# Kernel tuning notes

Measured on AMD Instinct MI355X. Metric: run time of the kernel, lower is better.

The kernel has to match this reference:

```python
import jax, jax.numpy as jnp
import numpy as np

N_NODES = 50000
N_EDGES = 800000
NUM_GRAPHS = 256
IN = 128
HID = 256
NUM_CLASSES = 10
EPS = 1e-5


def _glorot(key, shape):
    fan_in, fan_out = shape[0], shape[1]
    lim = (6.0 / (fan_in + fan_out)) ** 0.5
    return jax.random.uniform(key, shape, jnp.float32, -lim, lim)


def setup_inputs() -> dict:
    key = jax.random.key(0)
    ks = jax.random.split(key, 32)
    x = jax.random.normal(ks[0], (N_NODES, IN), jnp.float32)
    edge_index = jax.random.randint(ks[1], (2, N_EDGES), 0, N_NODES, jnp.int64)
    batch = jnp.sort(jax.random.randint(ks[2], (N_NODES,), 0, NUM_GRAPHS, jnp.int64))
    h = IN // 2  # 64
    p = {
        "x": x, "edge_index": edge_index, "batch": batch,
        # SAGEConv: out = lin_l(mean_aggr(x_j)) + lin_r(x_i); lin_l has bias, lin_r none
        "W1l": _glorot(ks[3], (IN, h)), "b1l": jnp.zeros((h,), jnp.float32), "W1r": _glorot(ks[4], (IN, h)),
        "W2l": _glorot(ks[5], (h, h)), "b2l": jnp.zeros((h,), jnp.float32), "W2r": _glorot(ks[6], (h, h)),
        "W3l": _glorot(ks[7], (h, h)), "b3l": jnp.zeros((h,), jnp.float32), "W3r": _glorot(ks[8], (h, h)),
        "lin1_w": _glorot(ks[9], (h, HID)), "lin1_b": jnp.zeros((HID,), jnp.float32),
        "g1": jnp.ones((HID,), jnp.float32), "be1": jnp.zeros((HID,), jnp.float32),
        "lin2_w": _glorot(ks[10], (HID, HID // 2)), "lin2_b": jnp.zeros((HID // 2,), jnp.float32),
        "g2": jnp.ones((HID // 2,), jnp.float32), "be2": jnp.zeros((HID // 2,), jnp.float32),
        "lin3_w": _glorot(ks[11], (HID // 2, HID // 4)), "lin3_b": jnp.zeros((HID // 4,), jnp.float32),
        "g3": jnp.ones((HID // 4,), jnp.float32), "be3": jnp.zeros((HID // 4,), jnp.float32),
        "lin4_w": _glorot(ks[12], (HID // 4, NUM_CLASSES)), "lin4_b": jnp.zeros((NUM_CLASSES,), jnp.float32),
    }
    return p


def sage_conv(x, src, dst, Wl, bl, Wr):
    # mean aggregation of source-node messages at destination nodes
    msg = x[src]  # [E, d] gather
    agg = jax.ops.segment_sum(msg, dst, num_segments=N_NODES)
    cnt = jax.ops.segment_sum(jnp.ones((src.shape[0],), x.dtype), dst, num_segments=N_NODES)
    agg = agg / jnp.maximum(cnt, 1.0)[:, None]
    return agg @ Wl + bl + x @ Wr


def batch_norm(x, gamma, beta):
    # training-mode BN (batch statistics, biased variance) as in torch default
    mean = jnp.mean(x, axis=0)
    var = jnp.mean((x - mean) ** 2, axis=0)
    return (x - mean) / jnp.sqrt(var + EPS) * gamma + beta


def reference(x, edge_index, batch,
              W1l, b1l, W1r, W2l, b2l, W2r, W3l, b3l, W3r,
              lin1_w, lin1_b, g1, be1, lin2_w, lin2_b, g2, be2,
              lin3_w, lin3_b, g3, be3, lin4_w, lin4_b):
    src, dst = edge_index[0], edge_index[1]
    h = sage_conv(x, src, dst, W1l, b1l, W1r)
    h = sage_conv(h, src, dst, W2l, b2l, W2r)
    h = sage_conv(h, src, dst, W3l, b3l, W3r)
    # global_mean_pool over graphs
    s = jax.ops.segment_sum(h, batch, num_segments=NUM_GRAPHS)
    n = jax.ops.segment_sum(jnp.ones((h.shape[0],), h.dtype), batch, num_segments=NUM_GRAPHS)
    c = s / jnp.maximum(n, 1.0)[:, None]
    # dropout is identity (self.training = False)
    c = jnp.tanh(batch_norm(c @ lin1_w + lin1_b, g1, be1))
    c = jnp.tanh(batch_norm(c @ lin2_w + lin2_b, g2, be2))
    c = jnp.tanh(batch_norm(c @ lin3_w + lin3_b, g3, be3))
    return c @ lin4_w + lin4_b
```

## Files before the change

### kernel.cpp

```cpp
#include <hip/hip_runtime.h>
#include <hip/hip_bf16.h>

#define N_NODES   50000
#define N_EDGES   800000
#define NUM_GRAPHS 256
#define IN_DIM    128
#define HD        64
#define EPS       1e-5f
#define SCAN_NB   196
#define NB_HEAD   64

typedef __hip_bfloat16 bf16;

__global__ void k_diag(float* __restrict__ out, int n, float v) {
    int t = blockIdx.x * 256 + threadIdx.x;
    if (t < n) out[t] = v;
}

__global__ void k_count(const int* __restrict__ dst, const int* __restrict__ batch,
                        int* __restrict__ cnti, int* __restrict__ pos,
                        int* __restrict__ gb) {
    int e = blockIdx.x * 256 + threadIdx.x;
    if (e < N_EDGES) pos[e] = atomicAdd(&cnti[dst[e]], 1);
    if (e < N_NODES) {
        int bg = batch[e];
        int bnext = (e + 1 < N_NODES) ? batch[e + 1] : NUM_GRAPHS;
        if (e == 0) {
            for (int g = 0; g <= bg; ++g) gb[g] = 0;
        }
        for (int g = bg + 1; g <= bnext; ++g) gb[g] = e + 1;
    }
}

__global__ void k_scan1(const int* __restrict__ cnti, int* __restrict__ off,
                        int* __restrict__ bsum) {
    __shared__ int wsum[4];
    int idx = blockIdx.x * 256 + threadIdx.x;
    int lane = threadIdx.x & 63, wid = threadIdx.x >> 6;
    int v = (idx < N_NODES) ? cnti[idx] : 0;
    int s = v;
    #pragma unroll
    for (int o = 1; o < 64; o <<= 1) {
        int u = __shfl_up(s, o);
        if (lane >= o) s += u;
    }
    if (lane == 63) wsum[wid] = s;
    __syncthreads();
    int wbase = 0;
    #pragma unroll
    for (int w = 0; w < 4; w++) wbase += (w < wid) ? wsum[w] : 0;
    if (idx < N_NODES) off[idx] = wbase + s - v;
    if (threadIdx.x == 255) bsum[blockIdx.x] = wbase + s;
}

__global__ void k_scan3(int* __restrict__ off, const int* __restrict__ bsum,
                        const int* __restrict__ gb, float* __restrict__ invc) {
    __shared__ int wsum[4];
    __shared__ int spre;
    int lane = threadIdx.x & 63, wid = threadIdx.x >> 6;
    int v = (threadIdx.x < blockIdx.x) ? bsum[threadIdx.x] : 0;
    #pragma unroll
    for (int o = 32; o > 0; o >>= 1) v += __shfl_down(v, o);
    if (lane == 0) wsum[wid] = v;
    __syncthreads();
    if (threadIdx.x == 0) spre = wsum[0] + wsum[1] + wsum[2] + wsum[3];
    __syncthreads();
    int pre = spre;
    int idx = blockIdx.x * 256 + threadIdx.x;
    if (idx < N_NODES) off[idx] += pre;
    else if (idx == N_NODES) off[N_NODES] = N_EDGES;
    if (blockIdx.x == 0 && threadIdx.x < NUM_GRAPHS) {
        int c0 = gb[threadIdx.x], c1 = gb[threadIdx.x + 1];
        invc[threadIdx.x] = 1.0f / (float)max(c1 - c0, 1);
    }
}

__global__ void k_fill(const int* __restrict__ src, const int* __restrict__ dst,
                       const int* __restrict__ off, const int* __restrict__ pos,
                       int* __restrict__ nbr) {
    int e = blockIdx.x * 256 + threadIdx.x;
    if (e >= N_EDGES) return;
    int d = dst[e];
    nbr[off[d] + pos[e]] = src[e];
}

template <int K>
__global__ __launch_bounds__(256) void k_xform3(
        const float* __restrict__ X, const float* __restrict__ Wl,
        const float* __restrict__ Wr, const float* __restrict__ bl,
        bf16* __restrict__ B, float* __restrict__ C) {
    __shared__ float tile[32 * K];
    const int NPW = 8;
    int nodes0 = blockIdx.x * 32;
    {
        const int total4 = 32 * K / 4;
        int nmax4 = (N_NODES - nodes0) * K / 4;
        const float4* Xg = (const float4*)(X + (long)nodes0 * K);
        float4* tg = (float4*)tile;
        for (int idx = threadIdx.x; idx < total4; idx += 256) {
            float4 v = make_float4(0.f, 0.f, 0.f, 0.f);
            if (idx < nmax4) v = Xg[idx];
            tg[idx] = v;
        }
    }
    __syncthreads();
    int wave = threadIdx.x >> 6, j = threadIdx.x & 63;
    long base = (long)nodes0 + wave * NPW;
    if (base >= N_NODES) return;
    float accB[NPW], accC[NPW];
    #pragma unroll
    for (int n = 0; n < NPW; n++) { accB[n] = 0.f; accC[n] = 0.f; }
    const float* Xs = tile + (wave * NPW) * K;
    for (int kc = 0; kc < K; kc += 4) {
        float wl0 = Wl[(kc + 0) * HD + j], wr0 = Wr[(kc + 0) * HD + j];
        float wl1 = Wl[(kc + 1) * HD + j], wr1 = Wr[(kc + 1) * HD + j];
        float wl2 = Wl[(kc + 2) * HD + j], wr2 = Wr[(kc + 2) * HD + j];
        float wl3 = Wl[(kc + 3) * HD + j], wr3 = Wr[(kc + 3) * HD + j];
        #pragma unroll
        for (int n = 0; n < NPW; n++) {
            float4 xv = *(const float4*)(Xs + n * K + kc);
            accB[n] = fmaf(xv.x, wl0, accB[n]);
            accC[n] = fmaf(xv.x, wr0, accC[n]);
            accB[n] = fmaf(xv.y, wl1, accB[n]);
            accC[n] = fmaf(xv.y, wr1, accC[n]);
            accB[n] = fmaf(xv.z, wl2, accB[n]);
            accC[n] = fmaf(xv.z, wr2, accC[n]);
            accB[n] = fmaf(xv.w, wl3, accB[n]);
            accC[n] = fmaf(xv.w, wr3, accC[n]);
        }
    }
    float bb = bl[j];
    int nact = (int)min((long)NPW, (long)N_NODES - base);
    for (int n = 0; n < nact; n++) {
        long i = base + n;
        B[i * HD + j] = __float2bfloat16(accB[n]);
        C[i * HD + j] = accC[n] + bb;
    }
}

__device__ __forceinline__ float bflo(unsigned u) { return __uint_as_float(u << 16); }
__device__ __forceinline__ float bfhi(unsigned u) { return __uint_as_float(u & 0xffff0000u); }

template <bool LAST>
__global__ void k_gather(const int* __restrict__ off, const int* __restrict__ nbr,
                         const bf16* __restrict__ Bm, float* __restrict__ C,
                         const int* __restrict__ batch, const float* __restrict__ invc,
                         float* __restrict__ cb) {
    int t = blockIdx.x * 256 + threadIdx.x;
    int i = t >> 6, lane = t & 63;
    if (!LAST && i >= N_NODES) return;
    int half = lane >> 5, c = lane & 31;
    int wid = threadIdx.x >> 6;
    const unsigned* B2 = (const unsigned*)Bm;
    int beg = off[i], end = off[i + 1];
    float e0 = 0.f, e1 = 0.f, e2 = 0.f, e3 = 0.f;
    float e4 = 0.f, e5 = 0.f, e6 = 0.f, e7 = 0.f;
    float o0 = 0.f, o1 = 0.f, o2 = 0.f, o3 = 0.f;
    float o4 = 0.f, o5 = 0.f, o6 = 0.f, o7 = 0.f;
    for (int base = beg; base < end; base += 64) {
        int idx = base + lane;
        int nv = (idx < end) ? nbr[idx] : 0;
        int m = min(64, end - base);
        int tt = 0;
        for (; tt + 16 <= m; tt += 16) {
            int n0 = __shfl(nv, tt + 0 + half);
            int n1 = __shfl(nv, tt + 2 + half);
            int n2 = __shfl(nv, tt + 4 + half);
            int n3 = __shfl(nv, tt + 6 + half);
            int n4 = __shfl(nv, tt + 8 + half);
            int n5 = __shfl(nv, tt + 10 + half);
            int n6 = __shfl(nv, tt + 12 + half);
            int n7 = __shfl(nv, tt + 14 + half);
            unsigned u0 = B2[(long)n0 * 32 + c];
            unsigned u1 = B2[(long)n1 * 32 + c];
            unsigned u2 = B2[(long)n2 * 32 + c];
            unsigned u3 = B2[(long)n3 * 32 + c];
            unsigned u4 = B2[(long)n4 * 32 + c];
            unsigned u5 = B2[(long)n5 * 32 + c];
            unsigned u6 = B2[(long)n6 * 32 + c];
            unsigned u7 = B2[(long)n7 * 32 + c];
            e0 += bflo(u0); o0 += bfhi(u0);
            e1 += bflo(u1); o1 += bfhi(u1);
            e2 += bflo(u2); o2 += bfhi(u2);
            e3 += bflo(u3); o3 += bfhi(u3);
            e4 += bflo(u4); o4 += bfhi(u4);
            e5 += bflo(u5); o5 += bfhi(u5);
            e6 += bflo(u6); o6 += bfhi(u6);
            e7 += bflo(u7); o7 += bfhi(u7);
        }
        for (; tt + 2 <= m; tt += 2) {
            int n0 = __shfl(nv, tt + half);
            unsigned u0 = B2[(long)n0 * 32 + c];
            e0 += bflo(u0); o0 += bfhi(u0);
        }
        if (tt < m) {
            int n0 = __shfl(nv, tt);
            if (half == 0) {
                unsigned u0 = B2[(long)n0 * 32 + c];
                e0 += bflo(u0); o0 += bfhi(u0);
            }
        }
    }
    float es = ((e0 + e1) + (e2 + e3)) + ((e4 + e5) + (e6 + e7));
    float os = ((o0 + o1) + (o2 + o3)) + ((o4 + o5) + (o6 + o7));
    es += __shfl(es, lane ^ 32);
    os += __shfl(os, lane ^ 32);
    if (!LAST) {
        if (half == 0) {
            int deg = end - beg;
            float inv = 1.0f / (float)max(deg, 1);
            float2* Cp = (float2*)(C + (long)i * HD + 2 * c);
            float2 cur = *Cp;
            cur.x += es * inv;
            cur.y += os * inv;
            *Cp = cur;
        }
    } else {
        __shared__ float red[4][64];
        __shared__ int gid[4];
        if (half == 0) {
            int deg = end - beg;
            float inv = 1.0f / (float)max(deg, 1);
            const float2 cur = *(const float2*)(C + (long)i * HD + 2 * c);
            red[wid][2 * c]     = cur.x + es * inv;
            red[wid][2 * c + 1] = cur.y + os * inv;
        }
        if (lane == 0) gid[wid] = batch[i];
        __syncthreads();
        if (wid == 0) {
            int g0 = gid[0], g1 = gid[1], g2 = gid[2], g3 = gid[3];
            float v0 = red[0][lane], v1 = red[1][lane];
            float v2 = red[2][lane], v3 = red[3][lane];
            if (g0 == g3) {
                atomicAdd(&cb[g0 * HD + lane],
                          ((v0 + v1) + (v2 + v3)) * invc[g0]);
            } else {
                atomicAdd(&cb[g0 * HD + lane], v0 * invc[g0]);
                atomicAdd(&cb[g1 * HD + lane], v1 * invc[g1]);
                atomicAdd(&cb[g2 * HD + lane], v2 * invc[g2]);
                atomicAdd(&cb[g3 * HD + lane], v3 * invc[g3]);
            }
        }
    }
}

__device__ __forceinline__ void gbar(int* bar, int round) {
    __syncthreads();
    if (threadIdx.x == 0) {
        __threadfence();
        __hip_atomic_fetch_add(bar, 1, __ATOMIC_RELEASE, __HIP_MEMORY_SCOPE_AGENT);
        int target = round * NB_HEAD;
        while (__hip_atomic_load(bar, __ATOMIC_ACQUIRE, __HIP_MEMORY_SCOPE_AGENT) < target) {}
        __threadfence();
    }
    __syncthreads();
}

template <int N, int K, int C>
__device__ __forceinline__ void lin_stage(
        const float* __restrict__ A, const float* __restrict__ W,
        const float* __restrict__ bia, const float* __restrict__ gam,
        const float* __restrict__ bet, float* __restrict__ out,
        float* s_sum, float* s_sq, float* s_m, float* s_sc) {
    const int NRG = 256 / C;
    int t = threadIdx.x;
    int jj = t & (C - 1);
    int rg = t / C;
    int j = blockIdx.x * C + jj;
    float vals[C];
    float bj = bia[j];
    #pragma unroll
    for (int i = 0; i < C; i++) vals[i] = bj;
    #pragma unroll 8
    for (int k = 0; k < K; k += 4) {
        float w0 = W[(k + 0) * N + j];
        float w1 = W[(k + 1) * N + j];
        float w2 = W[(k + 2) * N + j];
        float w3 = W[(k + 3) * N + j];
        #pragma unroll
        for (int i = 0; i < C; i++) {
            int r = rg + NRG * i;
            float4 a = *(const float4*)(A + r * K + k);
            vals[i] = fmaf(a.x, w0, vals[i]);
            vals[i] = fmaf(a.y, w1, vals[i]);
            vals[i] = fmaf(a.z, w2, vals[i]);
            vals[i] = fmaf(a.w, w3, vals[i]);
        }
    }
    float sum = 0.f, sq = 0.f;
    #pragma unroll
    for (int i = 0; i < C; i++) { sum += vals[i]; sq += vals[i] * vals[i]; }
    int lane = t & 63, wid = t >> 6;
    #pragma unroll
    for (int o = C; o < 64; o <<= 1) {
        sum += __shfl_xor(sum, o);
        sq  += __shfl_xor(sq, o);
    }
    if (lane < C) { s_sum[wid * C + lane] = sum; s_sq[wid * C + lane] = sq; }
    __syncthreads();
    if (t < C) {
        float S = s_sum[t] + s_sum[C + t] + s_sum[2 * C + t] + s_sum[3 * C + t];
        float Q = s_sq[t]  + s_sq[C + t]  + s_sq[2 * C + t]  + s_sq[3 * C + t];
        float mean = S * (1.0f / NUM_GRAPHS);
        float var = Q * (1.0f / NUM_GRAPHS) - mean * mean;
        s_m[t] = mean;
        s_sc[t] = rsqrtf(fmaxf(var, 0.f) + EPS) * gam[blockIdx.x * C + t];
    }
    __syncthreads();
    float mean = s_m[jj], sc = s_sc[jj], sh = bet[j];
    #pragma unroll
    for (int i = 0; i < C; i++) {
        out[(rg + NRG * i) * N + j] = tanhf((vals[i] - mean) * sc + sh);
    }
    __syncthreads();
}

__global__ __launch_bounds__(256) void k_head(
        int* bar,
        const float* __restrict__ l1w, const float* __restrict__ l1b,
        const float* __restrict__ g1, const float* __restrict__ be1,
        const float* __restrict__ l2w, const float* __restrict__ l2b,
        const float* __restrict__ g2, const float* __restrict__ be2,
        const float* __restrict__ l3w, const float* __restrict__ l3b,
        const float* __restrict__ g3, const float* __restrict__ be3,
        const float* __restrict__ w4, const float* __restrict__ b4,
        const float* __restrict__ cb, float* __restrict__ m1,
        float* __restrict__ m2, float* __restrict__ m3,
        float* __restrict__ out) {
    __shared__ float s_sum[16], s_sq[16], s_m[4], s_sc[4];
    int t = threadIdx.x;
    lin_stage<256, 64, 4>(cb, l1w, l1b, g1, be1, m1, s_sum, s_sq, s_m, s_sc);
    gbar(bar, 1);
    lin_stage<128, 256, 2>(m1, l2w, l2b, g2, be2, m2, s_sum, s_sq, s_m, s_sc);
    gbar(bar, 2);
    lin_stage<64, 128, 1>(m2, l3w, l3b, g3, be3, m3, s_sum, s_sq, s_m, s_sc);
    gbar(bar, 3);
    if (t < 40) {
        int q = t / 10, jf = t % 10;
        int row = blockIdx.x * 4 + q;
        const float* rp = m3 + row * 64;
        float s = b4[jf];
        #pragma unroll
        for (int k = 0; k < 64; k++) s = fmaf(rp[k], w4[k * 10 + jf], s);
        out[row * 10 + jf] = s;
    }
}

extern "C" void kernel_launch(void* const* d_in, const int* in_sizes, int n_in,
                              void* d_out, int out_size, void* d_ws, size_t ws_size,
                              hipStream_t stream) {
    const float* x     = (const float*)d_in[0];
    const int*   ei    = (const int*) d_in[1];
    const int*   batch = (const int*) d_in[2];
    const float *W1l = (const float*)d_in[3],  *b1l = (const float*)d_in[4],  *W1r = (const float*)d_in[5];
    const float *W2l = (const float*)d_in[6],  *b2l = (const float*)d_in[7],  *W2r = (const float*)d_in[8];
    const float *W3l = (const float*)d_in[9],  *b3l = (const float*)d_in[10], *W3r = (const float*)d_in[11];
    const float *lin1_w = (const float*)d_in[12], *lin1_b = (const float*)d_in[13];
    const float *g1 = (const float*)d_in[14], *be1 = (const float*)d_in[15];
    const float *lin2_w = (const float*)d_in[16], *lin2_b = (const float*)d_in[17];
    const float *g2 = (const float*)d_in[18], *be2 = (const float*)d_in[19];
    const float *lin3_w = (const float*)d_in[20], *lin3_b = (const float*)d_in[21];
    const float *g3 = (const float*)d_in[22], *be3 = (const float*)d_in[23];
    const float *lin4_w = (const float*)d_in[24], *lin4_b = (const float*)d_in[25];

    const int* srcp = ei;
    const int* dstp = ei + N_EDGES;

    const long NF = (long)N_NODES * HD;
    char* wsb  = (char*)d_ws;
    int*  cnti = (int*)wsb;
    int*  bar  = cnti + 50048;
    int*  pos  = bar  + 8;
    int*  off  = pos  + 800000;
    int*  nbr  = off  + 50056;
    int*  bsum = nbr  + 800000;
    int*  gb   = bsum + 256;
    float* invc = (float*)(gb + 264);
    bf16* B    = (bf16*)(invc + 256);
    float* H1  = (float*)(B + NF);
    float* H2  = H1  + NF;
    float* cb  = H2  + NF;
    float* m1  = cb  + NUM_GRAPHS * HD;
    float* m2  = m1  + NUM_GRAPHS * 256;
    float* m3  = m2  + NUM_GRAPHS * 128;
    float* endp= m3  + NUM_GRAPHS * 64;

    const size_t NEED = (size_t)((char*)endp - wsb);
    if (ws_size < NEED) {
        k_diag<<<(out_size + 255) / 256, 256, 0, stream>>>((float*)d_out, out_size,
                                                           (float)(ws_size >> 20));
        return;
    }

    const int TB = 256;
    const int gNE = (N_EDGES + TB - 1) / TB;
    const int gNF = (int)((NF + TB - 1) / TB);
    const int gXB = (N_NODES + 31) / 32;

    hipMemsetAsync(cnti, 0, (50048 + 8) * sizeof(int), stream);
    hipMemsetAsync(cb, 0, NUM_GRAPHS * HD * sizeof(float), stream);

    k_count<<<gNE, TB, 0, stream>>>(dstp, batch, cnti, pos, gb);
    k_scan1<<<SCAN_NB, TB, 0, stream>>>(cnti, off, bsum);
    k_scan3<<<SCAN_NB, TB, 0, stream>>>(off, bsum, gb, invc);
    k_fill<<<gNE, TB, 0, stream>>>(srcp, dstp, off, pos, nbr);

    k_xform3<IN_DIM><<<gXB, TB, 0, stream>>>(x, W1l, W1r, b1l, B, H1);
    k_gather<false><<<gNF, TB, 0, stream>>>(off, nbr, B, H1, batch, invc, cb);
    k_xform3<HD><<<gXB, TB, 0, stream>>>(H1, W2l, W2r, b2l, B, H2);
    k_gather<false><<<gNF, TB, 0, stream>>>(off, nbr, B, H2, batch, invc, cb);
    k_xform3<HD><<<gXB, TB, 0, stream>>>(H2, W3l, W3r, b3l, B, H1);
    k_gather<true><<<gNF, TB, 0, stream>>>(off, nbr, B, H1, batch, invc, cb);

    k_head<<<NB_HEAD, TB, 0, stream>>>(bar,
                                       lin1_w, lin1_b, g1, be1,
                                       lin2_w, lin2_b, g2, be2,
                                       lin3_w, lin3_b, g3, be3,
                                       lin4_w, lin4_b,
                                       cb, m1, m2, m3, (float*)d_out);
}
```

Baseline: 401.1 us.

## Partition MLP head by rows with atomic BN stats, keep activations in LDS

```diff
diff --git a/kernel.cpp b/kernel.cpp
--- a/kernel.cpp
+++ b/kernel.cpp
@@ -247,76 +247,19 @@
 __device__ __forceinline__ void gbar(int* bar, int round) {
     __syncthreads();
     if (threadIdx.x == 0) {
-        __threadfence();
-        __hip_atomic_fetch_add(bar, 1, __ATOMIC_RELEASE, __HIP_MEMORY_SCOPE_AGENT);
+        __hip_atomic_fetch_add(bar, 1, __ATOMIC_ACQ_REL, __HIP_MEMORY_SCOPE_AGENT);
         int target = round * NB_HEAD;
         while (__hip_atomic_load(bar, __ATOMIC_ACQUIRE, __HIP_MEMORY_SCOPE_AGENT) < target) {}
-        __threadfence();
-    }
-    __syncthreads();
-}
-
-template <int N, int K, int C>
-__device__ __forceinline__ void lin_stage(
-        const float* __restrict__ A, const float* __restrict__ W,
-        const float* __restrict__ bia, const float* __restrict__ gam,
-        const float* __restrict__ bet, float* __restrict__ out,
-        float* s_sum, float* s_sq, float* s_m, float* s_sc) {
-    const int NRG = 256 / C;
-    int t = threadIdx.x;
-    int jj = t & (C - 1);
-    int rg = t / C;
-    int j = blockIdx.x * C + jj;
-    float vals[C];
-    float bj = bia[j];
-    #pragma unroll
-    for (int i = 0; i < C; i++) vals[i] = bj;
-    #pragma unroll 8
-    for (int k = 0; k < K; k += 4) {
-        float w0 = W[(k + 0) * N + j];
-        float w1 = W[(k + 1) * N + j];
-        float w2 = W[(k + 2) * N + j];
-        float w3 = W[(k + 3) * N + j];
-        #pragma unroll
-        for (int i = 0; i < C; i++) {
-            int r = rg + NRG * i;
-            float4 a = *(const float4*)(A + r * K + k);
-            vals[i] = fmaf(a.x, w0, vals[i]);
-            vals[i] = fmaf(a.y, w1, vals[i]);
-            vals[i] = fmaf(a.z, w2, vals[i]);
-            vals[i] = fmaf(a.w, w3, vals[i]);
-        }
-    }
-    float sum = 0.f, sq = 0.f;
-    #pragma unroll
-    for (int i = 0; i < C; i++) { sum += vals[i]; sq += vals[i] * vals[i]; }
-    int lane = t & 63, wid = t >> 6;
-    #pragma unroll
-    for (int o = C; o < 64; o <<= 1) {
-        sum += __shfl_xor(sum, o);
-        sq  += __shfl_xor(sq, o);
-    }
-    if (lane < C) { s_sum[wid * C + lane] = sum; s_sq[wid * C + lane] = sq; }
-    __syncthreads();
-    if (t < C) {
-        float S = s_sum[t] + s_sum[C + t] + s_sum[2 * C + t] + s_sum[3 * C + t];
-        float Q = s_sq[t]  + s_sq[C + t]  + s_sq[2 * C + t]  + s_sq[3 * C + t];
-        float mean = S * (1.0f / NUM_GRAPHS);
-        float var = Q * (1.0f / NUM_GRAPHS) - mean * mean;
-        s_m[t] = mean;
-        s_sc[t] = rsqrtf(fmaxf(var, 0.f) + EPS) * gam[blockIdx.x * C + t];
-    }
-    __syncthreads();
-    float mean = s_m[jj], sc = s_sc[jj], sh = bet[j];
-    #pragma unroll
-    for (int i = 0; i < C; i++) {
-        out[(rg + NRG * i) * N + j] = tanhf((vals[i] - mean) * sc + sh);
-    }
-    __syncthreads();
+    }
+    __syncthreads();
+}
+
+__device__ __forceinline__ float ag_load(const float* p) {
+    return __hip_atomic_load(p, __ATOMIC_RELAXED, __HIP_MEMORY_SCOPE_AGENT);
 }
 
 __global__ __launch_bounds__(256) void k_head(
-        int* bar,
+        int* bar, float* __restrict__ gstat,
         const float* __restrict__ l1w, const float* __restrict__ l1b,
         const float* __restrict__ g1, const float* __restrict__ be1,
         const float* __restrict__ l2w, const float* __restrict__ l2b,
@@ -324,25 +267,115 @@
         const float* __restrict__ l3w, const float* __restrict__ l3b,
         const float* __restrict__ g3, const float* __restrict__ be3,
         const float* __restrict__ w4, const float* __restrict__ b4,
-        const float* __restrict__ cb, float* __restrict__ m1,
-        float* __restrict__ m2, float* __restrict__ m3,
-        float* __restrict__ out) {
-    __shared__ float s_sum[16], s_sq[16], s_m[4], s_sc[4];
+        const float* __restrict__ cb, float* __restrict__ out) {
+    __shared__ float A1[4][64];
+    __shared__ float A2[4][256];
+    __shared__ float A3[4][128];
+    __shared__ float M3[4][64];
+    float* gs1 = gstat;
+    float* gq1 = gstat + 256;
+    float* gs2 = gstat + 512;
+    float* gq2 = gstat + 640;
+    float* gs3 = gstat + 768;
+    float* gq3 = gstat + 832;
     int t = threadIdx.x;
-    lin_stage<256, 64, 4>(cb, l1w, l1b, g1, be1, m1, s_sum, s_sq, s_m, s_sc);
+    int r0 = blockIdx.x * 4;
+
+    {
+        int r = t >> 6, lane = t & 63;
+        A1[r][lane] = cb[(r0 + r) * HD + lane];
+    }
+    __syncthreads();
+
+    float v1[4];
+    {
+        int j = t;
+        float bj = l1b[j];
+        v1[0] = bj; v1[1] = bj; v1[2] = bj; v1[3] = bj;
+        #pragma unroll 4
+        for (int k = 0; k < 64; k++) {
+            float w = l1w[k * 256 + j];
+            v1[0] = fmaf(A1[0][k], w, v1[0]);
+            v1[1] = fmaf(A1[1][k], w, v1[1]);
+            v1[2] = fmaf(A1[2][k], w, v1[2]);
+            v1[3] = fmaf(A1[3][k], w, v1[3]);
+        }
+        float s = (v1[0] + v1[1]) + (v1[2] + v1[3]);
+        float q = (v1[0] * v1[0] + v1[1] * v1[1]) + (v1[2] * v1[2] + v1[3] * v1[3]);
+        atomicAdd(&gs1[j], s);
+        atomicAdd(&gq1[j], q);
+    }
     gbar(bar, 1);
-    lin_stage<128, 256, 2>(m1, l2w, l2b, g2, be2, m2, s_sum, s_sq, s_m, s_sc);
+    {
+        int j = t;
+        float S = ag_load(&gs1[j]), Q = ag_load(&gq1[j]);
+        float mean = S * (1.0f / NUM_GRAPHS);
+        float var = Q * (1.0f / NUM_GRAPHS) - mean * mean;
+        float sc = rsqrtf(fmaxf(var, 0.f) + EPS) * g1[j];
+        float sh = be1[j];
+        #pragma unroll
+        for (int r = 0; r < 4; r++)
+            A2[r][j] = tanhf((v1[r] - mean) * sc + sh);
+    }
+    __syncthreads();
+
+    float v2[2];
+    int j2 = t & 127, rq2 = t >> 7;
+    {
+        float bj = l2b[j2];
+        v2[0] = bj; v2[1] = bj;
+        #pragma unroll 4
+        for (int k = 0; k < 256; k++) {
+            float w = l2w[k * 128 + j2];
+            v2[0] = fmaf(A2[2 * rq2 + 0][k], w, v2[0]);
+            v2[1] = fmaf(A2[2 * rq2 + 1][k], w, v2[1]);
+        }
+        atomicAdd(&gs2[j2], v2[0] + v2[1]);
+        atomicAdd(&gq2[j2], v2[0] * v2[0] + v2[1] * v2[1]);
+    }
     gbar(bar, 2);
-    lin_stage<64, 128, 1>(m2, l3w, l3b, g3, be3, m3, s_sum, s_sq, s_m, s_sc);
+    {
+        float S = ag_load(&gs2[j2]), Q = ag_load(&gq2[j2]);
+        float mean = S * (1.0f / NUM_GRAPHS);
+        float var = Q * (1.0f / NUM_GRAPHS) - mean * mean;
+        float sc = rsqrtf(fmaxf(var, 0.f) + EPS) * g2[j2];
+        float sh = be2[j2];
+        A3[2 * rq2 + 0][j2] = tanhf((v2[0] - mean) * sc + sh);
+        A3[2 * rq2 + 1][j2] = tanhf((v2[1] - mean) * sc + sh);
+    }
+    __syncthreads();
+
+    float v3;
+    int j3 = t & 63, rq3 = t >> 6;
+    {
+        float bj = l3b[j3];
+        v3 = bj;
+        #pragma unroll 4
+        for (int k = 0; k < 128; k++) {
+            float w = l3w[k * 64 + j3];
+            v3 = fmaf(A3[rq3][k], w, v3);
+        }
+        atomicAdd(&gs3[j3], v3);
+        atomicAdd(&gq3[j3], v3 * v3);
+    }
     gbar(bar, 3);
+    {
+        float S = ag_load(&gs3[j3]), Q = ag_load(&gq3[j3]);
+        float mean = S * (1.0f / NUM_GRAPHS);
+        float var = Q * (1.0f / NUM_GRAPHS) - mean * mean;
+        float sc = rsqrtf(fmaxf(var, 0.f) + EPS) * g3[j3];
+        float sh = be3[j3];
+        M3[rq3][j3] = tanhf((v3 - mean) * sc + sh);
+    }
+    __syncthreads();
+
     if (t < 40) {
         int q = t / 10, jf = t % 10;
-        int row = blockIdx.x * 4 + q;
-        const float* rp = m3 + row * 64;
+        const float* rp = M3[q];
         float s = b4[jf];
         #pragma unroll
         for (int k = 0; k < 64; k++) s = fmaf(rp[k], w4[k * 10 + jf], s);
-        out[row * 10 + jf] = s;
+        out[(r0 + q) * 10 + jf] = s;
     }
 }
 
@@ -370,7 +403,8 @@
     char* wsb  = (char*)d_ws;
     int*  cnti = (int*)wsb;
     int*  bar  = cnti + 50048;
-    int*  pos  = bar  + 8;
+    float* gstat = (float*)(bar + 8);
+    int*  pos  = (int*)(gstat + 896);
     int*  off  = pos  + 800000;
     int*  nbr  = off  + 50056;
     int*  bsum = nbr  + 800000;
@@ -380,10 +414,7 @@
     float* H1  = (float*)(B + NF);
     float* H2  = H1  + NF;
     float* cb  = H2  + NF;
-    float* m1  = cb  + NUM_GRAPHS * HD;
-    float* m2  = m1  + NUM_GRAPHS * 256;
-    float* m3  = m2  + NUM_GRAPHS * 128;
-    float* endp= m3  + NUM_GRAPHS * 64;
+    float* endp= cb  + NUM_GRAPHS * HD;
 
     const size_t NEED = (size_t)((char*)endp - wsb);
     if (ws_size < NEED) {
@@ -397,7 +428,7 @@
     const int gNF = (int)((NF + TB - 1) / TB);
     const int gXB = (N_NODES + 31) / 32;
 
-    hipMemsetAsync(cnti, 0, (50048 + 8) * sizeof(int), stream);
+    hipMemsetAsync(cnti, 0, (50048 + 8 + 896) * sizeof(int), stream);
     hipMemsetAsync(cb, 0, NUM_GRAPHS * HD * sizeof(float), stream);
 
     k_count<<<gNE, TB, 0, stream>>>(dstp, batch, cnti, pos, gb);
@@ -412,10 +443,10 @@
     k_xform3<HD><<<gXB, TB, 0, stream>>>(H2, W3l, W3r, b3l, B, H1);
     k_gather<true><<<gNF, TB, 0, stream>>>(off, nbr, B, H1, batch, invc, cb);
 
-    k_head<<<NB_HEAD, TB, 0, stream>>>(bar,
+    k_head<<<NB_HEAD, TB, 0, stream>>>(bar, gstat,
                                        lin1_w, lin1_b, g1, be1,
                                        lin2_w, lin2_b, g2, be2,
                                        lin3_w, lin3_b, g3, be3,
                                        lin4_w, lin4_b,
-                                       cb, m1, m2, m3, (float*)d_out);
-}
+                                       cb, (float*)d_out);
+}
```

After: 395.6 us. About the same (-1.4%).
